# Kernel tuning notes

Measured on AMD Instinct MI355X. Metric: run time of the kernel, lower is better.

Reference implementation:

```python
import jax, jax.numpy as jnp
import numpy as np

B, T, U, D = 4, 320, 80, 512  # batch, enc frames, dec steps, per-stream dim
INNER, VOCAB, MAX_RLE = 512, 6, 50


def setup_inputs() -> dict:
    key = jax.random.key(0)
    ks = jax.random.split(key, 8)
    s = 0.02
    return {
        "enc_state": jax.random.normal(ks[0], (B, T, D), dtype=jnp.float32),
        "dec_state": jax.random.normal(ks[1], (B, U, D), dtype=jnp.float32),
        "W_f": jax.random.normal(ks[2], (INNER, 2 * D), dtype=jnp.float32) * s,
        "b_f": jax.random.normal(ks[3], (INNER,), dtype=jnp.float32) * s,
        "W_base": jax.random.normal(ks[4], (VOCAB, INNER), dtype=jnp.float32) * s,
        "b_base": jax.random.normal(ks[5], (VOCAB,), dtype=jnp.float32) * s,
        "W_rle": jax.random.normal(ks[6], (MAX_RLE, INNER), dtype=jnp.float32) * s,
        "b_rle": jax.random.normal(ks[7], (MAX_RLE,), dtype=jnp.float32) * s,
    }


def reference(enc_state, dec_state, W_f, b_f, W_base, b_base, W_rle, b_rle):
    # Tile enc [B,T,1,D] and dec [B,1,U,D] to [B,T,U,D] each, concat on last dim.
    t, u = enc_state.shape[1], dec_state.shape[1]
    enc = jnp.broadcast_to(enc_state[:, :, None, :], (enc_state.shape[0], t, u, enc_state.shape[-1]))
    dec = jnp.broadcast_to(dec_state[:, None, :, :], (dec_state.shape[0], t, u, dec_state.shape[-1]))
    concat = jnp.concatenate([enc, dec], axis=-1)  # [B,T,U,2D]
    h = jnp.tanh(jnp.einsum('btuk,ik->btui', concat, W_f) + b_f)  # [B,T,U,INNER]
    base_out = jnp.einsum('btui,vi->btuv', h, W_base) + b_base  # [B,T,U,VOCAB]
    rle_out = jnp.einsum('btui,ri->btur', h, W_rle) + b_rle      # [B,T,U,MAX_RLE]
    return (base_out, rle_out)
```

## Files before the change

### kernel.cpp

```cpp
#include <hip/hip_runtime.h>

typedef float f32x4 __attribute__((ext_vector_type(4)));
typedef short s16x8 __attribute__((ext_vector_type(8)));
typedef unsigned short u16;
typedef unsigned int u32;


__device__ __forceinline__ u16 f2bf(float f) {
  u32 u = __float_as_uint(f);
  u32 r = (u + 0x7FFFu + ((u >> 16) & 1u)) >> 16;
  return (u16)r;
}

__device__ __forceinline__ u32 cvt_pk_bf16(float lo, float hi) {
  u32 r;
  asm("v_cvt_pk_bf16_f32 %0, %1, %2" : "=v"(r) : "v"(lo), "v"(hi));
  return r;
}

__device__ __forceinline__ float fast_tanh(float x) {
  float e = __expf(2.f * x);
  return __builtin_fmaf(-2.f, __builtin_amdgcn_rcpf(e + 1.f), 1.f);
}

__device__ __forceinline__ void async16(const float* g, float* l) {
  __builtin_amdgcn_global_load_lds(
      (const __attribute__((address_space(1))) unsigned int*)g,
      (__attribute__((address_space(3))) unsigned int*)l, 16, 0, 0);
}

__global__ void prep_all(const float* __restrict__ enc, const float* __restrict__ dec,
                         s16x8* __restrict__ Xb,
                         const float* __restrict__ Wf, u16* __restrict__ WfF,
                         const float* __restrict__ Wb, const float* __restrict__ bb,
                         const float* __restrict__ Wr, const float* __restrict__ br,
                         u16* __restrict__ WoF, float* __restrict__ bias_cat) {
  int bx = blockIdx.x;
  int tid = threadIdx.x;
  if (bx < 400) {
    int idx = bx * 256 + tid;
    long e = (long)idx * 8;
    const float* src = (e < 655360) ? (enc + e) : (dec + (e - 655360));
    f32x4 a = *(const f32x4*)src;
    f32x4 b = *(const f32x4*)(src + 4);
    s16x8 o;
    o[0] = (short)f2bf(a[0]); o[1] = (short)f2bf(a[1]);
    o[2] = (short)f2bf(a[2]); o[3] = (short)f2bf(a[3]);
    o[4] = (short)f2bf(b[0]); o[5] = (short)f2bf(b[1]);
    o[6] = (short)f2bf(b[2]); o[7] = (short)f2bf(b[3]);
    Xb[idx] = o;
  } else if (bx < 2448) {
    int idx = (bx - 400) * 256 + tid;
    int j = idx & 7;
    int lane = (idx >> 3) & 63;
    int kk = (idx >> 9) & 15;
    int nt = (idx >> 13) & 31;
    int part = idx >> 18;
    int n = nt * 16 + (lane & 15);
    int k = part * 512 + kk * 32 + ((lane >> 4) << 3) + j;
    WfF[idx] = f2bf(Wf[n * 1024 + k]);
  } else {
    int idx = (bx - 2448) * 256 + tid;
    int j = idx & 7;
    int lane = (idx >> 3) & 63;
    int ks = (idx >> 9) & 15;
    int nt = idx >> 13;
    int v = nt * 16 + (lane & 15);
    int k = ks * 32 + ((lane >> 4) << 3) + j;
    float val = (v < 6) ? Wb[v * 512 + k] : (v < 56 ? Wr[(v - 6) * 512 + k] : 0.f);
    WoF[idx] = f2bf(val);
    if (bx == 2448 && tid < 64) {
      int vv = tid;
      bias_cat[vv] = (vv < 6) ? bb[vv] : (vv < 56 ? br[vv - 6] : 0.f);
    }
  }
}

__global__ __launch_bounds__(256) void egemm(const s16x8* __restrict__ Xb,
                                             const s16x8* __restrict__ WfF,
                                             const float* __restrict__ b_f,
                                             float* __restrict__ Ebf,
                                             float* __restrict__ Dc) {
  int ms = blockIdx.x >> 3;
  int ns = blockIdx.x & 7;
  int w = threadIdx.x >> 6, l = threadIdx.x & 63;
  int r0 = ms * 64 + w * 16;
  int part = (r0 >= 1280) ? 1 : 0;
  int n0 = ns * 64;
  int lrow = r0 + (l & 15);
  int khi = (l >> 4) << 3;
  f32x4 acc[4] = {};
#pragma unroll
  for (int kk = 0; kk < 16; ++kk) {
    s16x8 a = Xb[lrow * 64 + kk * 4 + (khi >> 3)];
#pragma unroll
    for (int nt = 0; nt < 4; ++nt) {
      int ntg = ns * 4 + nt;
      s16x8 bf = WfF[((part * 32 + ntg) * 16 + kk) * 64 + l];
      acc[nt] = __builtin_amdgcn_mfma_f32_16x16x32_bf16(a, bf, acc[nt], 0, 0, 0);
    }
  }
#pragma unroll
  for (int nt = 0; nt < 4; ++nt) {
    int n = n0 + nt * 16 + (l & 15);
    float bias = part ? 0.f : b_f[n];
#pragma unroll
    for (int q = 0; q < 4; ++q) {
      int row = r0 + ((l >> 4) << 2) + q;
      float val = acc[nt][q] + bias;
      if (part) Dc[(row - 1280) * 512 + n] = val;
      else      Ebf[row * 512 + n] = val;
    }
  }
}

template <int NRH>
__device__ __forceinline__ void jbody(float* dcbuf, u32* h_s,
                                      const float* __restrict__ Ebf,
                                      const float* __restrict__ Dc,
                                      const s16x8* __restrict__ WoF,
                                      const float* __restrict__ bias_cat,
                                      float* __restrict__ out, int bt0, int u0) {
  int b = bt0 / 320;
  const float* DcB = Dc + (long)(b * 80 + u0) * 512;
  const float* Eb0 = Ebf + (long)bt0 * 512;
  const float* Eb1 = Eb0 + 512;
  int tid = threadIdx.x, w = tid >> 6, l = tid & 63;
  int k4 = tid & 15;
  int v = w * 16 + (l & 15);
  float bias_v = bias_cat[v];
  f32x4 acc[2 * NRH];
#pragma unroll
  for (int i = 0; i < 2 * NRH; ++i) acc[i] = f32x4{0.f, 0.f, 0.f, 0.f};

#pragma unroll
  for (int r = 0; r < NRH; ++r) {
    int idx = tid + r * 256;
    async16(DcB + (idx >> 4) * 512 + (idx & 15) * 4, dcbuf + idx * 4);
  }
  __syncthreads();

#pragma unroll
  for (int c = 0; c < 8; ++c) {
    float* cur = dcbuf + (c & 1) * (NRH * 1024);
    if (c < 7) {
      float* nxt = dcbuf + ((c + 1) & 1) * (NRH * 1024);
#pragma unroll
      for (int r = 0; r < NRH; ++r) {
        int idx = tid + r * 256;
        async16(DcB + (idx >> 4) * 512 + (c + 1) * 64 + (idx & 15) * 4,
                nxt + idx * 4);
      }
    }
    s16x8 bfr0 = WoF[(w * 16 + c * 2 + 0) * 64 + l];
    s16x8 bfr1 = WoF[(w * 16 + c * 2 + 1) * 64 + l];
    f32x4 e0 = *(const f32x4*)(Eb0 + c * 64 + k4 * 4);
    f32x4 e1 = *(const f32x4*)(Eb1 + c * 64 + k4 * 4);

#pragma unroll
    for (int r2 = 0; r2 < 2 * NRH; ++r2) {
      int tt = r2 / NRH;
      int idx = tid + (r2 % NRH) * 256;
      int ul = idx >> 4;
      f32x4 d = *(const f32x4*)(cur + idx * 4);
      f32x4 e = tt ? e1 : e0;
      float t0 = fast_tanh(e[0] + d[0]);
      float t1 = fast_tanh(e[1] + d[1]);
      float t2 = fast_tanh(e[2] + d[2]);
      float t3 = fast_tanh(e[3] + d[3]);
      u32 lo = cvt_pk_bf16(t0, t1);
      u32 hi = cvt_pk_bf16(t2, t3);
      int row = tt * (NRH * 16) + ul;
      u32* hp = h_s + row * 32 + (((k4 >> 1) ^ (row & 7)) << 2) + (k4 & 1) * 2;
      hp[0] = lo; hp[1] = hi;
    }
    __syncthreads();

#pragma unroll
    for (int kk = 0; kk < 2; ++kk) {
      s16x8 bf = kk ? bfr1 : bfr0;
#pragma unroll
      for (int mt = 0; mt < 2 * NRH; ++mt) {
        int row = mt * 16 + (l & 15);
        int u16i = (kk * 4 + (l >> 4)) ^ (row & 7);
        s16x8 a = *(const s16x8*)(h_s + row * 32 + u16i * 4);
        acc[mt] = __builtin_amdgcn_mfma_f32_16x16x32_bf16(a, bf, acc[mt], 0, 0, 0);
      }
    }
    __syncthreads();
  }

#pragma unroll
  for (int mt = 0; mt < 2 * NRH; ++mt) {
    int tt = mt / NRH;
    long pbase = (long)(bt0 + tt) * 80 + u0 + (mt % NRH) * 16;
#pragma unroll
    for (int q = 0; q < 4; ++q) {
      int ur = ((l >> 4) << 2) + q;
      long p = pbase + ur;
      float val = acc[mt][q] + bias_v;
      if (v < 6)       out[p * 6 + v] = val;
      else if (v < 56) out[614400 + p * 50 + (v - 6)] = val;
    }
  }
}

__global__ __launch_bounds__(256) void joint_main(const float* __restrict__ Ebf,
                                                  const float* __restrict__ Dc,
                                                  const s16x8* __restrict__ WoF,
                                                  const float* __restrict__ bias_cat,
                                                  float* __restrict__ out) {
  __shared__ __align__(16) float dcbuf[2][3072];
  __shared__ __align__(16) u32 h_s[96 * 32];
  int bid = blockIdx.x;
  int bt0 = (bid >> 1) * 2;
  int half = bid & 1;
  if (half) jbody<2>(&dcbuf[0][0], h_s, Ebf, Dc, WoF, bias_cat, out, bt0, 48);
  else      jbody<3>(&dcbuf[0][0], h_s, Ebf, Dc, WoF, bias_cat, out, bt0, 0);
}

extern "C" void kernel_launch(void* const* d_in, const int* in_sizes, int n_in,
                              void* d_out, int out_size, void* d_ws, size_t ws_size,
                              hipStream_t stream) {
  (void)in_sizes; (void)n_in; (void)out_size; (void)ws_size;
  const float* enc = (const float*)d_in[0];
  const float* dec = (const float*)d_in[1];
  const float* Wf  = (const float*)d_in[2];
  const float* bf  = (const float*)d_in[3];
  const float* Wb  = (const float*)d_in[4];
  const float* bb  = (const float*)d_in[5];
  const float* Wr  = (const float*)d_in[6];
  const float* br  = (const float*)d_in[7];
  float* out = (float*)d_out;
  char* ws = (char*)d_ws;

  s16x8* Xb     = (s16x8*)(ws);
  u16*   WfF    = (u16*)(ws + 1638400);
  u16*   WoF    = (u16*)(ws + 2686976);
  float* biasC  = (float*)(ws + 2752512);
  float* Ebf    = (float*)(ws + 2752768);
  float* Dc     = (float*)(ws + 5374208);

  prep_all<<<2576, 256, 0, stream>>>(enc, dec, Xb, Wf, WfF, Wb, bb, Wr, br, WoF, biasC);
  egemm<<<200, 256, 0, stream>>>(Xb, (const s16x8*)WfF, bf, Ebf, Dc);
  joint_main<<<1280, 256, 0, stream>>>(Ebf, Dc, (const s16x8*)WoF, biasC, out);
}
```

Measured before the change: 50.23 us.

## Split joint kernel into uniform 16-step u tiles and double-buffer h tile

The joint kernel now handles one pair of encoder frames times 16 decoder steps per block, using a 3200-block grid instead of 1280 blocks split unevenly into 48 and 32 decoder steps. The per-block shared memory shrinks, which should raise occupancy and balance work across CUs. The tanh/bf16 h tile is double-buffered, so the trailing barrier in each K-chunk loop can be dropped. In exchange, each block loads the output weight fragments and encoder rows more times per output, since those are now reloaded for every 16-step tile.

New measurement: 47.23 us. -6.0%, faster.

```diff
diff --git a/kernel.cpp b/kernel.cpp
--- a/kernel.cpp
+++ b/kernel.cpp
@@ -114,64 +114,62 @@
   }
 }
 
-template <int NRH>
-__device__ __forceinline__ void jbody(float* dcbuf, u32* h_s,
-                                      const float* __restrict__ Ebf,
-                                      const float* __restrict__ Dc,
-                                      const s16x8* __restrict__ WoF,
-                                      const float* __restrict__ bias_cat,
-                                      float* __restrict__ out, int bt0, int u0) {
-  int b = bt0 / 320;
+__global__ __launch_bounds__(256) void joint_main(const float* __restrict__ Ebf,
+                                                  const float* __restrict__ Dc,
+                                                  const s16x8* __restrict__ WoF,
+                                                  const float* __restrict__ bias_cat,
+                                                  float* __restrict__ out) {
+  __shared__ __align__(16) float dcbuf[2][1024];
+  __shared__ __align__(16) u32 h_s[2][32 * 32];
+  int bid = blockIdx.x;
+  int pair = bid / 5, uf = bid - pair * 5;
+  int bt0 = pair * 2;
+  int b = pair / 160;
+  int u0 = uf * 16;
+  int tid = threadIdx.x, w = tid >> 6, l = tid & 63;
+  int k4 = tid & 15;
+  int row16 = tid >> 4;
+
   const float* DcB = Dc + (long)(b * 80 + u0) * 512;
   const float* Eb0 = Ebf + (long)bt0 * 512;
   const float* Eb1 = Eb0 + 512;
-  int tid = threadIdx.x, w = tid >> 6, l = tid & 63;
-  int k4 = tid & 15;
   int v = w * 16 + (l & 15);
   float bias_v = bias_cat[v];
-  f32x4 acc[2 * NRH];
-#pragma unroll
-  for (int i = 0; i < 2 * NRH; ++i) acc[i] = f32x4{0.f, 0.f, 0.f, 0.f};
-
-#pragma unroll
-  for (int r = 0; r < NRH; ++r) {
-    int idx = tid + r * 256;
-    async16(DcB + (idx >> 4) * 512 + (idx & 15) * 4, dcbuf + idx * 4);
-  }
+  f32x4 acc[2] = {};
+
+  async16(DcB + row16 * 512 + k4 * 4, &dcbuf[0][tid * 4]);
   __syncthreads();
 
 #pragma unroll
   for (int c = 0; c < 8; ++c) {
-    float* cur = dcbuf + (c & 1) * (NRH * 1024);
-    if (c < 7) {
-      float* nxt = dcbuf + ((c + 1) & 1) * (NRH * 1024);
-#pragma unroll
-      for (int r = 0; r < NRH; ++r) {
-        int idx = tid + r * 256;
-        async16(DcB + (idx >> 4) * 512 + (c + 1) * 64 + (idx & 15) * 4,
-                nxt + idx * 4);
-      }
-    }
+    float* cur = dcbuf[c & 1];
+    if (c < 7)
+      async16(DcB + row16 * 512 + (c + 1) * 64 + k4 * 4, &dcbuf[(c + 1) & 1][tid * 4]);
     s16x8 bfr0 = WoF[(w * 16 + c * 2 + 0) * 64 + l];
     s16x8 bfr1 = WoF[(w * 16 + c * 2 + 1) * 64 + l];
     f32x4 e0 = *(const f32x4*)(Eb0 + c * 64 + k4 * 4);
     f32x4 e1 = *(const f32x4*)(Eb1 + c * 64 + k4 * 4);
 
-#pragma unroll
-    for (int r2 = 0; r2 < 2 * NRH; ++r2) {
-      int tt = r2 / NRH;
-      int idx = tid + (r2 % NRH) * 256;
-      int ul = idx >> 4;
-      f32x4 d = *(const f32x4*)(cur + idx * 4);
-      f32x4 e = tt ? e1 : e0;
-      float t0 = fast_tanh(e[0] + d[0]);
-      float t1 = fast_tanh(e[1] + d[1]);
-      float t2 = fast_tanh(e[2] + d[2]);
-      float t3 = fast_tanh(e[3] + d[3]);
-      u32 lo = cvt_pk_bf16(t0, t1);
-      u32 hi = cvt_pk_bf16(t2, t3);
-      int row = tt * (NRH * 16) + ul;
-      u32* hp = h_s + row * 32 + (((k4 >> 1) ^ (row & 7)) << 2) + (k4 & 1) * 2;
+    f32x4 d = *(const f32x4*)(cur + tid * 4);
+    u32* hcur = h_s[c & 1];
+    {
+      float t0 = fast_tanh(e0[0] + d[0]);
+      float t1 = fast_tanh(e0[1] + d[1]);
+      float t2 = fast_tanh(e0[2] + d[2]);
+      float t3 = fast_tanh(e0[3] + d[3]);
+      u32 lo = cvt_pk_bf16(t0, t1), hi = cvt_pk_bf16(t2, t3);
+      int row = row16;
+      u32* hp = hcur + row * 32 + (((k4 >> 1) ^ (row & 7)) << 2) + (k4 & 1) * 2;
+      hp[0] = lo; hp[1] = hi;
+    }
+    {
+      float t0 = fast_tanh(e1[0] + d[0]);
+      float t1 = fast_tanh(e1[1] + d[1]);
+      float t2 = fast_tanh(e1[2] + d[2]);
+      float t3 = fast_tanh(e1[3] + d[3]);
+      u32 lo = cvt_pk_bf16(t0, t1), hi = cvt_pk_bf16(t2, t3);
+      int row = 16 + row16;
+      u32* hp = hcur + row * 32 + (((k4 >> 1) ^ (row & 7)) << 2) + (k4 & 1) * 2;
       hp[0] = lo; hp[1] = hi;
     }
     __syncthreads();
@@ -180,20 +178,18 @@
     for (int kk = 0; kk < 2; ++kk) {
       s16x8 bf = kk ? bfr1 : bfr0;
 #pragma unroll
-      for (int mt = 0; mt < 2 * NRH; ++mt) {
+      for (int mt = 0; mt < 2; ++mt) {
         int row = mt * 16 + (l & 15);
         int u16i = (kk * 4 + (l >> 4)) ^ (row & 7);
-        s16x8 a = *(const s16x8*)(h_s + row * 32 + u16i * 4);
+        s16x8 a = *(const s16x8*)(hcur + row * 32 + u16i * 4);
         acc[mt] = __builtin_amdgcn_mfma_f32_16x16x32_bf16(a, bf, acc[mt], 0, 0, 0);
       }
     }
-    __syncthreads();
-  }
-
-#pragma unroll
-  for (int mt = 0; mt < 2 * NRH; ++mt) {
-    int tt = mt / NRH;
-    long pbase = (long)(bt0 + tt) * 80 + u0 + (mt % NRH) * 16;
+  }
+
+#pragma unroll
+  for (int mt = 0; mt < 2; ++mt) {
+    long pbase = (long)(bt0 + mt) * 80 + u0;
 #pragma unroll
     for (int q = 0; q < 4; ++q) {
       int ur = ((l >> 4) << 2) + q;
@@ -203,20 +199,6 @@
       else if (v < 56) out[614400 + p * 50 + (v - 6)] = val;
     }
   }
-}
-
-__global__ __launch_bounds__(256) void joint_main(const float* __restrict__ Ebf,
-                                                  const float* __restrict__ Dc,
-                                                  const s16x8* __restrict__ WoF,
-                                                  const float* __restrict__ bias_cat,
-                                                  float* __restrict__ out) {
-  __shared__ __align__(16) float dcbuf[2][3072];
-  __shared__ __align__(16) u32 h_s[96 * 32];
-  int bid = blockIdx.x;
-  int bt0 = (bid >> 1) * 2;
-  int half = bid & 1;
-  if (half) jbody<2>(&dcbuf[0][0], h_s, Ebf, Dc, WoF, bias_cat, out, bt0, 48);
-  else      jbody<3>(&dcbuf[0][0], h_s, Ebf, Dc, WoF, bias_cat, out, bt0, 0);
 }
 
 extern "C" void kernel_launch(void* const* d_in, const int* in_sizes, int n_in,
@@ -243,5 +225,5 @@
 
   prep_all<<<2576, 256, 0, stream>>>(enc, dec, Xb, Wf, WfF, Wb, bb, Wr, br, WoF, biasC);
   egemm<<<200, 256, 0, stream>>>(Xb, (const s16x8*)WfF, bf, Ebf, Dc);
-  joint_main<<<1280, 256, 0, stream>>>(Ebf, Dc, (const s16x8*)WoF, biasC, out);
-}
+  joint_main<<<3200, 256, 0, stream>>>(Ebf, Dc, (const s16x8*)WoF, biasC, out);
+}
```
